# Optimization experiments

Measured on AMD Instinct MI355X. Metric: run time of the kernel, lower is better.

## Reference

```python
import jax, jax.numpy as jnp
import numpy as np
from jax import lax

NUM_CLASSES = 19
IGNORE_INDEX = 255
THRESH = 0.7
MIN_KEPT = 100000

N, C, H, W = 8, 19, 512, 1024


def setup_inputs() -> dict:
    key = jax.random.key(0)
    k1, k2 = jax.random.split(key)
    predict = jax.random.normal(k1, (N, C, H, W), dtype=jnp.float32)
    target = jax.random.randint(k2, (N, H, W), 0, NUM_CLASSES, dtype=jnp.int32)
    return {"predict": predict, "target": target}


def _class_weights(flat_lab):
    # get_weights: median(counts)/counts for present classes, 1.0 otherwise.
    ones = jnp.ones(flat_lab.shape, dtype=jnp.float32)
    counts = jnp.zeros((NUM_CLASSES,), jnp.float32).at[flat_lab].add(ones, mode='drop')
    present = counts > 0
    med = jnp.nanmedian(jnp.where(present, counts, jnp.nan))
    return jnp.where(present, med / jnp.maximum(counts, 1.0), 1.0)


def reference(predict, target):
    n, c, h, w = predict.shape
    flat_lab = target.reshape(-1)                       # (P,)
    valid = flat_lab != IGNORE_INDEX                    # (P,)
    num_valid = valid.sum()

    weight = _class_weights(flat_lab)                   # (C,) from ORIGINAL target

    # per-pixel log-softmax over classes
    logits = jnp.transpose(predict, (0, 2, 3, 1)).reshape(-1, c)  # (P, C)
    logp = jax.nn.log_softmax(logits, axis=-1)
    safe_lab = jnp.where(valid, flat_lab, 0)
    logp_true = jnp.take_along_axis(logp, safe_lab[:, None], axis=1)[:, 0]  # (P,)
    pred_prob = jnp.exp(lax.stop_gradient(logp_true))   # prob of true class, detached

    # order-statistic threshold over valid pixels (invalid -> +inf, sorts last)
    pred_sortable = jnp.where(valid, pred_prob, jnp.inf)
    sorted_pred = jnp.sort(pred_sortable)
    k = jnp.minimum(MIN_KEPT, num_valid) - 1
    kth = sorted_pred[jnp.maximum(k, 0)]
    threshold = jnp.where(kth > THRESH, kth, THRESH)

    kept_ohem = valid & (pred_sortable <= threshold)
    do_ohem = num_valid > MIN_KEPT                      # else keep all valid pixels
    kept = jnp.where(do_ohem, kept_ohem, valid)

    # weighted cross entropy over kept pixels (torch 'mean' with class weights)
    wpix = weight[safe_lab] * kept.astype(jnp.float32)
    loss = jnp.sum(wpix * (-logp_true)) / jnp.maximum(jnp.sum(wpix), 1e-12)
    return loss
```

## Files before the change

### kernel.cpp

```cpp
#include <hip/hip_runtime.h>

#define NCLS 19
#define HW_ (512 * 1024)
#define MIN_KEPT_ 100000LL
#define NSLOT 32
#define COARSE_BINS 1280
#define COARSE_BASE 0x3F333u

struct Accums {
    unsigned int coarse[COARSE_BINS];
    unsigned int fine12[4096];
    unsigned int slotCnt[NSLOT][NCLS];
    float        slotSumA[NSLOT][NCLS];
    unsigned int slotCnt07[NSLOT][NCLS];
    float        slotSum07[NSLOT][NCLS];
    unsigned int cntR[NCLS];
    float        sumR[NCLS];
    float        weights[NCLS];
    unsigned int flag;
    unsigned int sel_prefix;
    unsigned int rank_rem;
    float        threshold;
};

__device__ __forceinline__ void accum_pixel(unsigned int* sCnt, float* sSumA,
                                            unsigned int* sCnt07, float* sSum07,
                                            Accums* ws, int lab, float logp, float prob) {
    if (lab < 0 || lab >= NCLS) return;
    float nlp = -logp;
    atomicAdd(&sCnt[lab], 1u);
    atomicAdd(&sSumA[lab], nlp);
    if (prob <= 0.7f) {
        atomicAdd(&sCnt07[lab], 1u);
        atomicAdd(&sSum07[lab], nlp);
    } else {
        unsigned int bits = __float_as_uint(prob);
        int bin = (int)(bits >> 12) - (int)COARSE_BASE;
        bin = bin < 0 ? 0 : (bin >= COARSE_BINS ? COARSE_BINS - 1 : bin);
        atomicAdd(&ws->coarse[bin], 1u);
    }
}

__device__ __forceinline__ bool pix_logp(const float* __restrict__ pred,
                                         const int* __restrict__ targ,
                                         int p, float& logp, float& prob, int& lab) {
    lab = targ[p];
    if (lab < 0 || lab >= NCLS) return false;
    int n = p / HW_;
    int hw = p - n * HW_;
    const float* pb = pred + (size_t)n * NCLS * HW_ + hw;
    float v[NCLS];
    float mx = -3.4e38f, vt = 0.f;
#pragma unroll
    for (int c = 0; c < NCLS; ++c) {
        float x = pb[(size_t)c * HW_];
        v[c] = x;
        mx = fmaxf(mx, x);
        vt = (lab == c) ? x : vt;
    }
    float s = 0.f;
#pragma unroll
    for (int c = 0; c < NCLS; ++c) s += __expf(v[c] - mx);
    logp = vt - (mx + __logf(s));
    prob = __expf(logp);
    return true;
}

__global__ __launch_bounds__(256) void k_main(const float* __restrict__ pred,
                                              const int* __restrict__ targ,
                                              Accums* __restrict__ ws, int P) {
    __shared__ unsigned int sCnt[NCLS], sCnt07[NCLS];
    __shared__ float sSumA[NCLS], sSum07[NCLS];
    if (threadIdx.x < NCLS) {
        sCnt[threadIdx.x] = 0u; sCnt07[threadIdx.x] = 0u;
        sSumA[threadIdx.x] = 0.f; sSum07[threadIdx.x] = 0.f;
    }
    __syncthreads();

    int gid = blockIdx.x * blockDim.x + threadIdx.x;
    int p4 = gid * 4;
    if (p4 < P) {
        if (p4 + 3 < P) {
            int n = p4 / HW_;
            int hw = p4 - n * HW_;
            const float* pb = pred + (size_t)n * NCLS * HW_ + hw;
            int4 lab = *reinterpret_cast<const int4*>(targ + p4);
            float4 vv[NCLS];
            float4 mx = make_float4(-3.4e38f, -3.4e38f, -3.4e38f, -3.4e38f);
            float4 vt = make_float4(0.f, 0.f, 0.f, 0.f);
#pragma unroll
            for (int c = 0; c < NCLS; ++c) {
                float4 v = *reinterpret_cast<const float4*>(pb + (size_t)c * HW_);
                vv[c] = v;
                mx.x = fmaxf(mx.x, v.x); mx.y = fmaxf(mx.y, v.y);
                mx.z = fmaxf(mx.z, v.z); mx.w = fmaxf(mx.w, v.w);
                vt.x = (lab.x == c) ? v.x : vt.x;
                vt.y = (lab.y == c) ? v.y : vt.y;
                vt.z = (lab.z == c) ? v.z : vt.z;
                vt.w = (lab.w == c) ? v.w : vt.w;
            }
            float4 s = make_float4(0.f, 0.f, 0.f, 0.f);
#pragma unroll
            for (int c = 0; c < NCLS; ++c) {
                s.x += __expf(vv[c].x - mx.x);
                s.y += __expf(vv[c].y - mx.y);
                s.z += __expf(vv[c].z - mx.z);
                s.w += __expf(vv[c].w - mx.w);
            }
            {
                float lp = vt.x - (mx.x + __logf(s.x));
                accum_pixel(sCnt, sSumA, sCnt07, sSum07, ws, lab.x, lp, __expf(lp));
                lp = vt.y - (mx.y + __logf(s.y));
                accum_pixel(sCnt, sSumA, sCnt07, sSum07, ws, lab.y, lp, __expf(lp));
                lp = vt.z - (mx.z + __logf(s.z));
                accum_pixel(sCnt, sSumA, sCnt07, sSum07, ws, lab.z, lp, __expf(lp));
                lp = vt.w - (mx.w + __logf(s.w));
                accum_pixel(sCnt, sSumA, sCnt07, sSum07, ws, lab.w, lp, __expf(lp));
            }
        } else {
            for (int j = 0; j < 4; ++j) {
                int p = p4 + j;
                if (p >= P) break;
                float lp, pr; int lb;
                if (pix_logp(pred, targ, p, lp, pr, lb))
                    accum_pixel(sCnt, sSumA, sCnt07, sSum07, ws, lb, lp, pr);
            }
        }
    }
    __syncthreads();
    int slot = blockIdx.x & (NSLOT - 1);
    if (threadIdx.x < NCLS) {
        int i = threadIdx.x;
        if (sCnt[i])          atomicAdd(&ws->slotCnt[slot][i], sCnt[i]);
        if (sSumA[i] != 0.f)  atomicAdd(&ws->slotSumA[slot][i], sSumA[i]);
        if (sCnt07[i])        atomicAdd(&ws->slotCnt07[slot][i], sCnt07[i]);
        if (sSum07[i] != 0.f) atomicAdd(&ws->slotSum07[slot][i], sSum07[i]);
    }
}

__global__ void k_finalize(Accums* __restrict__ ws, float* __restrict__ out) {
    __shared__ unsigned int cnt[NCLS], c07[NCLS];
    __shared__ float sA[NCLS], s07[NCLS];
    int t = threadIdx.x;
    if (t < NCLS) {
        unsigned int c = 0, c7 = 0; float a = 0.f, b = 0.f;
        for (int s = 0; s < NSLOT; ++s) {
            c  += ws->slotCnt[s][t];   a += ws->slotSumA[s][t];
            c7 += ws->slotCnt07[s][t]; b += ws->slotSum07[s][t];
        }
        cnt[t] = c; c07[t] = c7; sA[t] = a; s07[t] = b;
    }
    __syncthreads();
    if (t != 0) return;

    long long nv = 0, c7tot = 0;
    for (int c = 0; c < NCLS; ++c) { nv += cnt[c]; c7tot += c07[c]; }

    float w[NCLS];
    {
        float vals[NCLS]; int m = 0;
        for (int c = 0; c < NCLS; ++c)
            if (cnt[c] > 0) vals[m++] = (float)cnt[c];
        for (int i = 1; i < m; ++i) {
            float x = vals[i]; int j = i - 1;
            while (j >= 0 && vals[j] > x) { vals[j + 1] = vals[j]; --j; }
            vals[j + 1] = x;
        }
        float med = 1.f;
        if (m > 0) med = (m & 1) ? vals[m / 2] : 0.5f * (vals[m / 2 - 1] + vals[m / 2]);
        for (int c = 0; c < NCLS; ++c) {
            w[c] = (cnt[c] > 0) ? med / fmaxf((float)cnt[c], 1.f) : 1.f;
            ws->weights[c] = w[c];
        }
    }

    if (nv == 0) { out[0] = 0.f; return; }

    bool do_ohem = nv > MIN_KEPT_;
    long long kkeep = nv < MIN_KEPT_ ? nv : MIN_KEPT_;

    float S = 0.f, W = 0.f;
    if (!do_ohem) {
        for (int c = 0; c < NCLS; ++c) { S += w[c] * sA[c]; W += w[c] * (float)cnt[c]; }
    } else if (c7tot >= kkeep) {
        for (int c = 0; c < NCLS; ++c) { S += w[c] * s07[c]; W += w[c] * (float)c07[c]; }
    } else {
        unsigned int r = (unsigned int)(kkeep - c7tot);
        unsigned int cum = 0, before = 0; int bsel = COARSE_BINS - 1;
        for (int i = 0; i < COARSE_BINS; ++i) {
            unsigned int nc = cum + ws->coarse[i];
            if (nc >= r) { bsel = i; before = cum; break; }
            cum = nc;
        }
        ws->sel_prefix = COARSE_BASE + (unsigned int)bsel;
        ws->rank_rem = r - before;
        ws->flag = 1u;
        return;
    }
    out[0] = S / fmaxf(W, 1e-12f);
}

__global__ void k_refine(const float* __restrict__ pred, const int* __restrict__ targ,
                         Accums* __restrict__ ws, int P) {
    __shared__ unsigned int flag; __shared__ unsigned int prefix;
    if (threadIdx.x == 0) { flag = ws->flag; prefix = ws->sel_prefix; }
    __syncthreads();
    if (!flag) return;
    int stride = gridDim.x * blockDim.x;
    for (int p = blockIdx.x * blockDim.x + threadIdx.x; p < P; p += stride) {
        float lp, pr; int lb;
        if (!pix_logp(pred, targ, p, lp, pr, lb)) continue;
        if (pr > 0.7f) {
            unsigned int bits = __float_as_uint(pr);
            if ((bits >> 12) == prefix) atomicAdd(&ws->fine12[bits & 0xFFFu], 1u);
        }
    }
}

__global__ void k_pick(Accums* __restrict__ ws) {
    if (threadIdx.x != 0) return;
    if (!ws->flag) return;
    unsigned int r = ws->rank_rem, cum = 0, low = 4095;
    for (unsigned int i = 0; i < 4096; ++i) {
        cum += ws->fine12[i];
        if (cum >= r) { low = i; break; }
    }
    ws->threshold = __uint_as_float((ws->sel_prefix << 12) | low);
}

__global__ void k_rare_accum(const float* __restrict__ pred, const int* __restrict__ targ,
                             Accums* __restrict__ ws, int P) {
    __shared__ unsigned int flag; __shared__ float thr;
    if (threadIdx.x == 0) { flag = ws->flag; thr = ws->threshold; }
    __syncthreads();
    if (!flag) return;
    int stride = gridDim.x * blockDim.x;
    for (int p = blockIdx.x * blockDim.x + threadIdx.x; p < P; p += stride) {
        float lp, pr; int lb;
        if (!pix_logp(pred, targ, p, lp, pr, lb)) continue;
        if (pr <= thr) {
            atomicAdd(&ws->cntR[lb], 1u);
            atomicAdd(&ws->sumR[lb], -lp);
        }
    }
}

__global__ void k_rare_final(Accums* __restrict__ ws, float* __restrict__ out) {
    if (threadIdx.x != 0) return;
    if (!ws->flag) return;
    float S = 0.f, W = 0.f;
    for (int c = 0; c < NCLS; ++c) {
        S += ws->weights[c] * ws->sumR[c];
        W += ws->weights[c] * (float)ws->cntR[c];
    }
    out[0] = S / fmaxf(W, 1e-12f);
}

extern "C" void kernel_launch(void* const* d_in, const int* in_sizes, int n_in,
                              void* d_out, int out_size, void* d_ws, size_t ws_size,
                              hipStream_t stream) {
    const float* pred = (const float*)d_in[0];
    const int*   targ = (const int*)d_in[1];
    float*       out  = (float*)d_out;
    int P = in_sizes[1];
    Accums* ws = (Accums*)d_ws;

    hipMemsetAsync(d_ws, 0, sizeof(Accums), stream);
    hipMemsetAsync(d_out, 0, (size_t)out_size * sizeof(float), stream);

    int blocks = (P + 1023) / 1024;
    k_main<<<blocks, 256, 0, stream>>>(pred, targ, ws, P);
    k_finalize<<<1, 64, 0, stream>>>(ws, out);
    k_refine<<<2048, 256, 0, stream>>>(pred, targ, ws, P);
    k_pick<<<1, 64, 0, stream>>>(ws);
    k_rare_accum<<<2048, 256, 0, stream>>>(pred, targ, ws, P);
    k_rare_final<<<1, 64, 0, stream>>>(ws, out);
}
```

Before: 458.8 us.

## Fold pick and final kernels into last-block epilogues and drop output memset

The tiny k_pick and k_rare_final kernels become last-block-done epilogues inside k_refine and k_rare, using atomic done counters. This cuts launches from six to four and removes the output memset. k_main now counts pixels with prob above 0.7 instead of below, and finalize derives the below-threshold counts and sums by subtraction. The refine and rare grids shrink to 1024 blocks. In the common path the flag is probably zero, so the refine/rare kernels exit early and the saving is mostly launch overhead. Dropping the memset relies on finalize or rare always writing out.

Measured after the change: 447.2 us. -2.5%, faster.

```diff
diff --git a/kernel.cpp b/kernel.cpp
--- a/kernel.cpp
+++ b/kernel.cpp
@@ -12,8 +12,8 @@
     unsigned int fine12[4096];
     unsigned int slotCnt[NSLOT][NCLS];
     float        slotSumA[NSLOT][NCLS];
-    unsigned int slotCnt07[NSLOT][NCLS];
-    float        slotSum07[NSLOT][NCLS];
+    unsigned int slotCntG[NSLOT][NCLS];
+    float        slotSumG[NSLOT][NCLS];
     unsigned int cntR[NCLS];
     float        sumR[NCLS];
     float        weights[NCLS];
@@ -21,19 +21,26 @@
     unsigned int sel_prefix;
     unsigned int rank_rem;
     float        threshold;
+    unsigned int done1, done2;
 };
 
+__device__ __forceinline__ unsigned int aloadu(const unsigned int* p) {
+    return __hip_atomic_load(p, __ATOMIC_RELAXED, __HIP_MEMORY_SCOPE_AGENT);
+}
+__device__ __forceinline__ float aloadf(const float* p) {
+    return __hip_atomic_load(p, __ATOMIC_RELAXED, __HIP_MEMORY_SCOPE_AGENT);
+}
+
 __device__ __forceinline__ void accum_pixel(unsigned int* sCnt, float* sSumA,
-                                            unsigned int* sCnt07, float* sSum07,
+                                            unsigned int* sCntG, float* sSumG,
                                             Accums* ws, int lab, float logp, float prob) {
     if (lab < 0 || lab >= NCLS) return;
     float nlp = -logp;
     atomicAdd(&sCnt[lab], 1u);
     atomicAdd(&sSumA[lab], nlp);
-    if (prob <= 0.7f) {
-        atomicAdd(&sCnt07[lab], 1u);
-        atomicAdd(&sSum07[lab], nlp);
-    } else {
+    if (prob > 0.7f) {
+        atomicAdd(&sCntG[lab], 1u);
+        atomicAdd(&sSumG[lab], nlp);
         unsigned int bits = __float_as_uint(prob);
         int bin = (int)(bits >> 12) - (int)COARSE_BASE;
         bin = bin < 0 ? 0 : (bin >= COARSE_BINS ? COARSE_BINS - 1 : bin);
@@ -69,11 +76,11 @@
 __global__ __launch_bounds__(256) void k_main(const float* __restrict__ pred,
                                               const int* __restrict__ targ,
                                               Accums* __restrict__ ws, int P) {
-    __shared__ unsigned int sCnt[NCLS], sCnt07[NCLS];
-    __shared__ float sSumA[NCLS], sSum07[NCLS];
+    __shared__ unsigned int sCnt[NCLS], sCntG[NCLS];
+    __shared__ float sSumA[NCLS], sSumG[NCLS];
     if (threadIdx.x < NCLS) {
-        sCnt[threadIdx.x] = 0u; sCnt07[threadIdx.x] = 0u;
-        sSumA[threadIdx.x] = 0.f; sSum07[threadIdx.x] = 0.f;
+        sCnt[threadIdx.x] = 0u; sCntG[threadIdx.x] = 0u;
+        sSumA[threadIdx.x] = 0.f; sSumG[threadIdx.x] = 0.f;
     }
     __syncthreads();
 
@@ -109,13 +116,13 @@
             }
             {
                 float lp = vt.x - (mx.x + __logf(s.x));
-                accum_pixel(sCnt, sSumA, sCnt07, sSum07, ws, lab.x, lp, __expf(lp));
+                accum_pixel(sCnt, sSumA, sCntG, sSumG, ws, lab.x, lp, __expf(lp));
                 lp = vt.y - (mx.y + __logf(s.y));
-                accum_pixel(sCnt, sSumA, sCnt07, sSum07, ws, lab.y, lp, __expf(lp));
+                accum_pixel(sCnt, sSumA, sCntG, sSumG, ws, lab.y, lp, __expf(lp));
                 lp = vt.z - (mx.z + __logf(s.z));
-                accum_pixel(sCnt, sSumA, sCnt07, sSum07, ws, lab.z, lp, __expf(lp));
+                accum_pixel(sCnt, sSumA, sCntG, sSumG, ws, lab.z, lp, __expf(lp));
                 lp = vt.w - (mx.w + __logf(s.w));
-                accum_pixel(sCnt, sSumA, sCnt07, sSum07, ws, lab.w, lp, __expf(lp));
+                accum_pixel(sCnt, sSumA, sCntG, sSumG, ws, lab.w, lp, __expf(lp));
             }
         } else {
             for (int j = 0; j < 4; ++j) {
@@ -123,7 +130,7 @@
                 if (p >= P) break;
                 float lp, pr; int lb;
                 if (pix_logp(pred, targ, p, lp, pr, lb))
-                    accum_pixel(sCnt, sSumA, sCnt07, sSum07, ws, lb, lp, pr);
+                    accum_pixel(sCnt, sSumA, sCntG, sSumG, ws, lb, lp, pr);
             }
         }
     }
@@ -133,28 +140,28 @@
         int i = threadIdx.x;
         if (sCnt[i])          atomicAdd(&ws->slotCnt[slot][i], sCnt[i]);
         if (sSumA[i] != 0.f)  atomicAdd(&ws->slotSumA[slot][i], sSumA[i]);
-        if (sCnt07[i])        atomicAdd(&ws->slotCnt07[slot][i], sCnt07[i]);
-        if (sSum07[i] != 0.f) atomicAdd(&ws->slotSum07[slot][i], sSum07[i]);
+        if (sCntG[i])         atomicAdd(&ws->slotCntG[slot][i], sCntG[i]);
+        if (sSumG[i] != 0.f)  atomicAdd(&ws->slotSumG[slot][i], sSumG[i]);
     }
 }
 
 __global__ void k_finalize(Accums* __restrict__ ws, float* __restrict__ out) {
-    __shared__ unsigned int cnt[NCLS], c07[NCLS];
-    __shared__ float sA[NCLS], s07[NCLS];
+    __shared__ unsigned int cnt[NCLS], cG[NCLS];
+    __shared__ float sA[NCLS], sG[NCLS];
     int t = threadIdx.x;
     if (t < NCLS) {
-        unsigned int c = 0, c7 = 0; float a = 0.f, b = 0.f;
+        unsigned int c = 0, cg = 0; float a = 0.f, b = 0.f;
         for (int s = 0; s < NSLOT; ++s) {
-            c  += ws->slotCnt[s][t];   a += ws->slotSumA[s][t];
-            c7 += ws->slotCnt07[s][t]; b += ws->slotSum07[s][t];
-        }
-        cnt[t] = c; c07[t] = c7; sA[t] = a; s07[t] = b;
+            c  += ws->slotCnt[s][t];  a += ws->slotSumA[s][t];
+            cg += ws->slotCntG[s][t]; b += ws->slotSumG[s][t];
+        }
+        cnt[t] = c; cG[t] = cg; sA[t] = a; sG[t] = b;
     }
     __syncthreads();
     if (t != 0) return;
 
     long long nv = 0, c7tot = 0;
-    for (int c = 0; c < NCLS; ++c) { nv += cnt[c]; c7tot += c07[c]; }
+    for (int c = 0; c < NCLS; ++c) { nv += cnt[c]; c7tot += (long long)(cnt[c] - cG[c]); }
 
     float w[NCLS];
     {
@@ -183,7 +190,10 @@
     if (!do_ohem) {
         for (int c = 0; c < NCLS; ++c) { S += w[c] * sA[c]; W += w[c] * (float)cnt[c]; }
     } else if (c7tot >= kkeep) {
-        for (int c = 0; c < NCLS; ++c) { S += w[c] * s07[c]; W += w[c] * (float)c07[c]; }
+        for (int c = 0; c < NCLS; ++c) {
+            S += w[c] * (sA[c] - sG[c]);
+            W += w[c] * (float)(cnt[c] - cG[c]);
+        }
     } else {
         unsigned int r = (unsigned int)(kkeep - c7tot);
         unsigned int cum = 0, before = 0; int bsel = COARSE_BINS - 1;
@@ -202,7 +212,7 @@
 
 __global__ void k_refine(const float* __restrict__ pred, const int* __restrict__ targ,
                          Accums* __restrict__ ws, int P) {
-    __shared__ unsigned int flag; __shared__ unsigned int prefix;
+    __shared__ unsigned int flag; __shared__ unsigned int prefix; __shared__ int sIsLast;
     if (threadIdx.x == 0) { flag = ws->flag; prefix = ws->sel_prefix; }
     __syncthreads();
     if (!flag) return;
@@ -215,22 +225,27 @@
             if ((bits >> 12) == prefix) atomicAdd(&ws->fine12[bits & 0xFFFu], 1u);
         }
     }
-}
-
-__global__ void k_pick(Accums* __restrict__ ws) {
-    if (threadIdx.x != 0) return;
-    if (!ws->flag) return;
-    unsigned int r = ws->rank_rem, cum = 0, low = 4095;
-    for (unsigned int i = 0; i < 4096; ++i) {
-        cum += ws->fine12[i];
-        if (cum >= r) { low = i; break; }
-    }
-    ws->threshold = __uint_as_float((ws->sel_prefix << 12) | low);
-}
-
-__global__ void k_rare_accum(const float* __restrict__ pred, const int* __restrict__ targ,
-                             Accums* __restrict__ ws, int P) {
-    __shared__ unsigned int flag; __shared__ float thr;
+    __syncthreads();
+    if (threadIdx.x == 0) {
+        __threadfence();
+        unsigned int old = __hip_atomic_fetch_add(&ws->done1, 1u, __ATOMIC_ACQ_REL,
+                                                  __HIP_MEMORY_SCOPE_AGENT);
+        sIsLast = (old == gridDim.x - 1);
+    }
+    __syncthreads();
+    if (sIsLast && threadIdx.x == 0) {
+        unsigned int r = ws->rank_rem, cum = 0, low = 4095;
+        for (unsigned int i = 0; i < 4096; ++i) {
+            cum += aloadu(&ws->fine12[i]);
+            if (cum >= r) { low = i; break; }
+        }
+        ws->threshold = __uint_as_float((prefix << 12) | low);
+    }
+}
+
+__global__ void k_rare(const float* __restrict__ pred, const int* __restrict__ targ,
+                       Accums* __restrict__ ws, float* __restrict__ out, int P) {
+    __shared__ unsigned int flag; __shared__ float thr; __shared__ int sIsLast;
     if (threadIdx.x == 0) { flag = ws->flag; thr = ws->threshold; }
     __syncthreads();
     if (!flag) return;
@@ -243,17 +258,22 @@
             atomicAdd(&ws->sumR[lb], -lp);
         }
     }
-}
-
-__global__ void k_rare_final(Accums* __restrict__ ws, float* __restrict__ out) {
-    if (threadIdx.x != 0) return;
-    if (!ws->flag) return;
-    float S = 0.f, W = 0.f;
-    for (int c = 0; c < NCLS; ++c) {
-        S += ws->weights[c] * ws->sumR[c];
-        W += ws->weights[c] * (float)ws->cntR[c];
-    }
-    out[0] = S / fmaxf(W, 1e-12f);
+    __syncthreads();
+    if (threadIdx.x == 0) {
+        __threadfence();
+        unsigned int old = __hip_atomic_fetch_add(&ws->done2, 1u, __ATOMIC_ACQ_REL,
+                                                  __HIP_MEMORY_SCOPE_AGENT);
+        sIsLast = (old == gridDim.x - 1);
+    }
+    __syncthreads();
+    if (sIsLast && threadIdx.x == 0) {
+        float S = 0.f, W = 0.f;
+        for (int c = 0; c < NCLS; ++c) {
+            S += ws->weights[c] * aloadf(&ws->sumR[c]);
+            W += ws->weights[c] * (float)aloadu(&ws->cntR[c]);
+        }
+        out[0] = S / fmaxf(W, 1e-12f);
+    }
 }
 
 extern "C" void kernel_launch(void* const* d_in, const int* in_sizes, int n_in,
@@ -266,13 +286,10 @@
     Accums* ws = (Accums*)d_ws;
 
     hipMemsetAsync(d_ws, 0, sizeof(Accums), stream);
-    hipMemsetAsync(d_out, 0, (size_t)out_size * sizeof(float), stream);
 
     int blocks = (P + 1023) / 1024;
     k_main<<<blocks, 256, 0, stream>>>(pred, targ, ws, P);
     k_finalize<<<1, 64, 0, stream>>>(ws, out);
-    k_refine<<<2048, 256, 0, stream>>>(pred, targ, ws, P);
-    k_pick<<<1, 64, 0, stream>>>(ws);
-    k_rare_accum<<<2048, 256, 0, stream>>>(pred, targ, ws, P);
-    k_rare_final<<<1, 64, 0, stream>>>(ws, out);
-}
+    k_refine<<<1024, 256, 0, stream>>>(pred, targ, ws, P);
+    k_rare<<<1024, 256, 0, stream>>>(pred, targ, ws, out, P);
+}
```
